# Optimization experiments

Measured on AMD Instinct MI355X. Metric: run time of the kernel, lower is better.

Reference implementation:

```python
import jax, jax.numpy as jnp
import numpy as np

N = 1 << 20        # number of query points
L_HIDDEN = 6       # hidden (64->64) layers, i.e. params[1:-1]
NEG_SLOPE = 0.2    # nn.LeakyReLU(0.2)

# NOTE: nn.Dropout(0.5) is treated in eval mode (identity), the standard
# convention for deterministic correctness baselines.

def _lrelu(x):
    return jnp.where(x >= 0, x, NEG_SLOPE * x)


def setup_inputs() -> dict:
    key = jax.random.key(0)
    ks = jax.random.split(key, 11)
    return {
        "points": jax.random.normal(ks[0], (N, 3), jnp.float32),
        "w0": jax.random.normal(ks[1], (3, 64), jnp.float32),
        "s0": jax.random.normal(ks[2], (64,), jnp.float32),
        "b0": jax.random.normal(ks[3], (64,), jnp.float32),
        "wh": jax.random.normal(ks[4], (L_HIDDEN, 64, 64), jnp.float32),
        "sh": jax.random.normal(ks[5], (L_HIDDEN, 64), jnp.float32),
        "bh": jax.random.normal(ks[6], (L_HIDDEN, 64), jnp.float32),
        "wo": jax.random.normal(ks[7], (64, 1), jnp.float32),
        "so": jax.random.normal(ks[8], (), jnp.float32),
        "bo": jax.random.normal(ks[9], (), jnp.float32),
    }


def reference(points, w0, s0, b0, wh, sh, bh, wo, so, bo):
    # first layer: [N,3] @ [3,64] * scale + bias -> leakyrelu
    x = _lrelu(jnp.matmul(points, w0) * s0 + b0)
    # hidden layers: small static loop over structurally distinct param sets
    for i in range(L_HIDDEN):
        x = _lrelu(jnp.matmul(x, wh[i]) * sh[i] + bh[i])
    # output layer: [N,64] @ [64,1] * scalar + scalar (no activation)
    return jnp.matmul(x, wo) * so + bo
```

## Files before the change

### kernel.cpp

```cpp
#include <hip/hip_runtime.h>


typedef _Float16 half8 __attribute__((ext_vector_type(8)));
typedef _Float16 half2v __attribute__((ext_vector_type(2)));
typedef float floatx16 __attribute__((ext_vector_type(16)));
typedef float float2v __attribute__((ext_vector_type(2)));

#define N_HID 6
#define OFF_A 0
#define OFF_B 49152
#define OFF_C 51200
#define OFF_D 52992
#define SETUP_TOTAL (24576 + 1024 + 448 + 64)

__global__ __launch_bounds__(256) void setup_weights(
    const float* __restrict__ w0, const float* __restrict__ s0, const float* __restrict__ b0,
    const float* __restrict__ wh, const float* __restrict__ sh, const float* __restrict__ bh,
    const float* __restrict__ wo, const float* __restrict__ so,
    unsigned char* __restrict__ ws)
{
    int i = blockIdx.x * 256 + threadIdx.x;
    if (i < 24576) {
        int j = i & 7, lane = (i >> 3) & 63, s = (i >> 9) & 3, t = (i >> 11) & 1, l = i >> 12;
        int m = 32 * t + (lane & 31);
        int h = lane >> 5;
        int feat = 16 * s + 8 * (j >> 2) + 4 * h + (j & 3);
        ((_Float16*)(ws + OFF_A))[i] = (_Float16)(wh[(l * 64 + feat) * 64 + m] * sh[l * 64 + m]);
    } else if (i < 24576 + 1024) {
        int i2 = i - 24576;
        int j = i2 & 7, lane = (i2 >> 3) & 63, t = i2 >> 9;
        int m = 32 * t + (lane & 31);
        int k = 8 * (lane >> 5) + j;
        float v = (k < 3) ? w0[k * 64 + m] * s0[m] * 0.015625f
                          : (k == 3 ? b0[m] * 0.015625f : 0.f);
        ((_Float16*)(ws + OFF_B))[i2] = (_Float16)v;
    } else if (i < 24576 + 1024 + 448) {
        int i2 = i - 24576 - 1024;
        int r = i2 & 15, t = (i2 >> 4) & 1, h = (i2 >> 5) & 1, l = i2 >> 6;
        int feat = 32 * t + (r & 3) + 8 * ((r >> 2) & 3) + 4 * h;
        float bv = (l == 0) ? b0[feat] : bh[(l - 1) * 64 + feat];
        ((float*)(ws + OFF_C))[i2] = bv * 0.015625f;
    } else if (i < SETUP_TOTAL) {
        int i2 = i - 24576 - 1024 - 448;
        int r = i2 & 15, t = (i2 >> 4) & 1, h = i2 >> 5;
        int feat = 32 * t + (r & 3) + 8 * ((r >> 2) & 3) + 4 * h;
        ((float*)(ws + OFF_D))[i2] = wo[feat] * so[0] * 64.f;
    }
}

union FragU { int i[4]; half8 v; };

static __device__ __forceinline__ int pkrtz(float a, float b) {
    auto hh = __builtin_amdgcn_cvt_pkrtz(a, b);
    int r;
    __builtin_memcpy(&r, &hh, 4);
    return r;
}

static __device__ __forceinline__ int lrelu2(int v) {
    half2v u;
    __builtin_memcpy(&u, &v, 4);
    half2v w = u * (_Float16)0.2f;
    half2v r = __builtin_elementwise_max(u, w);
    int o;
    __builtin_memcpy(&o, &r, 4);
    return o;
}

static __device__ __forceinline__ floatx16 mfma16(half8 a, half8 b, floatx16 c) {
    return __builtin_amdgcn_mfma_f32_32x32x16_f16(a, b, c, 0, 0, 0);
}

__global__ __launch_bounds__(64, 1) void mlp_mfma(
    const float* __restrict__ points,
    const unsigned char* __restrict__ ws,
    const float* __restrict__ bhg,
    const float* __restrict__ bo,
    float* __restrict__ out, int n)
{
    const int lane = threadIdx.x;
    const int p = lane & 31;
    const int h = lane >> 5;

    half8 Wreg[N_HID][2][4];
    {
        const half8* WfG = (const half8*)(ws + OFF_A);
#pragma unroll
        for (int l = 0; l < N_HID; ++l)
#pragma unroll
            for (int t = 0; t < 2; ++t)
#pragma unroll
                for (int s = 0; s < 4; ++s)
                    Wreg[l][t][s] = WfG[(((l * 2 + t) * 4 + s) << 6) + lane];
    }
    half8 W0a, W0b;
    {
        const half8* A0g = (const half8*)(ws + OFF_B);
        W0a = A0g[lane];
        W0b = A0g[64 + lane];
    }
    half8 biasF[N_HID][2];
#pragma unroll
    for (int l = 0; l < N_HID; ++l)
#pragma unroll
        for (int t = 0; t < 2; ++t) {
            FragU u;
            u.i[0] = u.i[1] = u.i[2] = u.i[3] = 0;
            if (h == 0) u.v[0] = (_Float16)(bhg[l * 64 + 32 * t + p] * 0.015625f);
            biasF[l][t] = u.v;
        }
    half8 oneF;
    {
        FragU u;
        u.i[0] = u.i[1] = u.i[2] = u.i[3] = 0;
        if (h == 0) u.v[0] = (_Float16)1.0f;
        oneF = u.v;
    }
    floatx16 wo0, wo1;
    {
        const floatx16* woG = (const floatx16*)(ws + OFF_D);
        wo0 = woG[h * 2 + 0];
        wo1 = woG[h * 2 + 1];
    }
    const float bov = bo[0];

    const int nbatch = (n + 63) >> 6;
    int b = blockIdx.x;
    if (b >= nbatch) return;

    float P0x, P0y, P0z, P1x, P1y, P1z;
    {
        int q0 = min(b * 64 + p, n - 1), q1 = min(b * 64 + 32 + p, n - 1);
        P0x = points[3 * q0]; P0y = points[3 * q0 + 1]; P0z = points[3 * q0 + 2];
        P1x = points[3 * q1]; P1y = points[3 * q1 + 1]; P1z = points[3 * q1 + 2];
    }

    while (true) {
        const int nb = b + (int)gridDim.x;
        const bool more = nb < nbatch;
        float N0x, N0y, N0z, N1x, N1y, N1z;
        N0x = N0y = N0z = N1x = N1y = N1z = 0.f;
        if (more) {
            int q0 = min(nb * 64 + p, n - 1), q1 = min(nb * 64 + 32 + p, n - 1);
            N0x = points[3 * q0]; N0y = points[3 * q0 + 1]; N0z = points[3 * q0 + 2];
            N1x = points[3 * q1]; N1y = points[3 * q1 + 1]; N1z = points[3 * q1 + 2];
        }

        floatx16 acc0[2], acc1[2];
        {
            FragU bu0, bu1;
            bu0.i[0] = bu0.i[1] = bu0.i[2] = bu0.i[3] = 0;
            bu1 = bu0;
            if (h == 0) {
                bu0.v[0] = (_Float16)P0x; bu0.v[1] = (_Float16)P0y;
                bu0.v[2] = (_Float16)P0z; bu0.v[3] = (_Float16)1.0f;
                bu1.v[0] = (_Float16)P1x; bu1.v[1] = (_Float16)P1y;
                bu1.v[2] = (_Float16)P1z; bu1.v[3] = (_Float16)1.0f;
            }
            acc0[0] = mfma16(W0a, bu0.v, (floatx16)(0.0f));
            acc0[1] = mfma16(W0b, bu0.v, (floatx16)(0.0f));
            acc1[0] = mfma16(W0a, bu1.v, (floatx16)(0.0f));
            acc1[1] = mfma16(W0b, bu1.v, (floatx16)(0.0f));
        }

#pragma unroll
        for (int l = 0; l < N_HID; ++l) {
            floatx16 bc0 = mfma16(biasF[l][0], oneF, (floatx16)(0.0f));
            floatx16 bc1 = mfma16(biasF[l][1], oneF, (floatx16)(0.0f));
            floatx16 n00, n01, n10, n11;
#pragma unroll
            for (int s = 0; s < 4; ++s) {
                const int t = s >> 1, rpb = 4 * (s & 1);
                FragU f0, f1;
#pragma unroll
                for (int c = 0; c < 4; ++c) {
                    f0.i[c] = lrelu2(pkrtz(acc0[t][2 * (rpb + c)], acc0[t][2 * (rpb + c) + 1]));
                    f1.i[c] = lrelu2(pkrtz(acc1[t][2 * (rpb + c)], acc1[t][2 * (rpb + c) + 1]));
                }
                if (s == 0) {
                    n00 = mfma16(Wreg[l][0][0], f0.v, bc0);
                    n01 = mfma16(Wreg[l][1][0], f0.v, bc1);
                    n10 = mfma16(Wreg[l][0][0], f1.v, bc0);
                    n11 = mfma16(Wreg[l][1][0], f1.v, bc1);
                } else {
                    n00 = mfma16(Wreg[l][0][s], f0.v, n00);
                    n01 = mfma16(Wreg[l][1][s], f0.v, n01);
                    n10 = mfma16(Wreg[l][0][s], f1.v, n10);
                    n11 = mfma16(Wreg[l][1][s], f1.v, n11);
                }
            }
            acc0[0] = n00; acc0[1] = n01; acc1[0] = n10; acc1[1] = n11;
        }

        {
            float2v q0 = {0.f, 0.f}, q1 = {0.f, 0.f};
#pragma unroll
            for (int r2 = 0; r2 < 8; ++r2) {
                float2v w0p = { wo0[2 * r2], wo0[2 * r2 + 1] };
                float2v w1p = { wo1[2 * r2], wo1[2 * r2 + 1] };
                float2v u;
                u.x = acc0[0][2 * r2]; u.y = acc0[0][2 * r2 + 1];
                u = __builtin_elementwise_max(u, 0.2f * u);
                q0 += u * w0p;
                u.x = acc0[1][2 * r2]; u.y = acc0[1][2 * r2 + 1];
                u = __builtin_elementwise_max(u, 0.2f * u);
                q0 += u * w1p;
                u.x = acc1[0][2 * r2]; u.y = acc1[0][2 * r2 + 1];
                u = __builtin_elementwise_max(u, 0.2f * u);
                q1 += u * w0p;
                u.x = acc1[1][2 * r2]; u.y = acc1[1][2 * r2 + 1];
                u = __builtin_elementwise_max(u, 0.2f * u);
                q1 += u * w1p;
            }
            float part0 = q0.x + q0.y;
            float part1 = q1.x + q1.y;
            part0 += __shfl_xor(part0, 32);
            part1 += __shfl_xor(part1, 32);
            if (h == 0) {
                int pt0 = b * 64 + p, pt1 = b * 64 + 32 + p;
                if (pt0 < n) out[pt0] = part0 + bov;
                if (pt1 < n) out[pt1] = part1 + bov;
            }
        }

        if (!more) break;
        P0x = N0x; P0y = N0y; P0z = N0z;
        P1x = N1x; P1y = N1y; P1z = N1z;
        b = nb;
    }
}

extern "C" void kernel_launch(void* const* d_in, const int* in_sizes, int n_in,
                              void* d_out, int out_size, void* d_ws, size_t ws_size,
                              hipStream_t stream) {
    const float* points = (const float*)d_in[0];
    const float* w0     = (const float*)d_in[1];
    const float* s0     = (const float*)d_in[2];
    const float* b0     = (const float*)d_in[3];
    const float* wh     = (const float*)d_in[4];
    const float* sh     = (const float*)d_in[5];
    const float* bh     = (const float*)d_in[6];
    const float* wo     = (const float*)d_in[7];
    const float* so     = (const float*)d_in[8];
    const float* bo     = (const float*)d_in[9];

    const int n = in_sizes[0] / 3;

    setup_weights<<<(SETUP_TOTAL + 255) / 256, 256, 0, stream>>>(
        w0, s0, b0, wh, sh, bh, wo, so, (unsigned char*)d_ws);

    mlp_mfma<<<1024, 64, 0, stream>>>(
        points, (const unsigned char*)d_ws, bh, bo, (float*)d_out, n);
}
```

Baseline: 143.2 us.

## Pack hidden biases into two MFMA fragments and run two waves per SIMD

Replaces the twelve per-layer bias fragments held in registers with two packed fp16 fragments built in setup, one element per layer. Each layer selects its bias column through a one-hot B fragment in the bias MFMA. This frees VGPRs so launch bounds can ask for two waves per SIMD, and the grid doubles to 2048 blocks to fill them. The risk is register pressure or spills with the tighter bound, since all hidden-layer weights stay resident in registers.

Measured after the change: 199.8 us. 39.6% more time.

```diff
diff --git a/kernel.cpp b/kernel.cpp
--- a/kernel.cpp
+++ b/kernel.cpp
@@ -9,9 +9,9 @@
 #define N_HID 6
 #define OFF_A 0
 #define OFF_B 49152
-#define OFF_C 51200
-#define OFF_D 52992
-#define SETUP_TOTAL (24576 + 1024 + 448 + 64)
+#define OFF_E 51200
+#define OFF_D 53248
+#define SETUP_TOTAL (24576 + 1024 + 1024 + 64)
 
 __global__ __launch_bounds__(256) void setup_weights(
     const float* __restrict__ w0, const float* __restrict__ s0, const float* __restrict__ b0,
@@ -34,14 +34,15 @@
         float v = (k < 3) ? w0[k * 64 + m] * s0[m] * 0.015625f
                           : (k == 3 ? b0[m] * 0.015625f : 0.f);
         ((_Float16*)(ws + OFF_B))[i2] = (_Float16)v;
-    } else if (i < 24576 + 1024 + 448) {
+    } else if (i < 24576 + 2048) {
         int i2 = i - 24576 - 1024;
-        int r = i2 & 15, t = (i2 >> 4) & 1, h = (i2 >> 5) & 1, l = i2 >> 6;
-        int feat = 32 * t + (r & 3) + 8 * ((r >> 2) & 3) + 4 * h;
-        float bv = (l == 0) ? b0[feat] : bh[(l - 1) * 64 + feat];
-        ((float*)(ws + OFF_C))[i2] = bv * 0.015625f;
+        int j = i2 & 7, lane = (i2 >> 3) & 63, t = i2 >> 9;
+        int m = 32 * t + (lane & 31);
+        int h = lane >> 5;
+        float v = (h == 0 && j < N_HID) ? bh[j * 64 + m] * 0.015625f : 0.f;
+        ((_Float16*)(ws + OFF_E))[i2] = (_Float16)v;
     } else if (i < SETUP_TOTAL) {
-        int i2 = i - 24576 - 1024 - 448;
+        int i2 = i - 24576 - 2048;
         int r = i2 & 15, t = (i2 >> 4) & 1, h = i2 >> 5;
         int feat = 32 * t + (r & 3) + 8 * ((r >> 2) & 3) + 4 * h;
         ((float*)(ws + OFF_D))[i2] = wo[feat] * so[0] * 64.f;
@@ -71,10 +72,9 @@
     return __builtin_amdgcn_mfma_f32_32x32x16_f16(a, b, c, 0, 0, 0);
 }
 
-__global__ __launch_bounds__(64, 1) void mlp_mfma(
+__global__ __launch_bounds__(64, 2) void mlp_mfma(
     const float* __restrict__ points,
     const unsigned char* __restrict__ ws,
-    const float* __restrict__ bhg,
     const float* __restrict__ bo,
     float* __restrict__ out, int n)
 {
@@ -99,22 +99,11 @@
         W0a = A0g[lane];
         W0b = A0g[64 + lane];
     }
-    half8 biasF[N_HID][2];
-#pragma unroll
-    for (int l = 0; l < N_HID; ++l)
-#pragma unroll
-        for (int t = 0; t < 2; ++t) {
-            FragU u;
-            u.i[0] = u.i[1] = u.i[2] = u.i[3] = 0;
-            if (h == 0) u.v[0] = (_Float16)(bhg[l * 64 + 32 * t + p] * 0.015625f);
-            biasF[l][t] = u.v;
-        }
-    half8 oneF;
-    {
-        FragU u;
-        u.i[0] = u.i[1] = u.i[2] = u.i[3] = 0;
-        if (h == 0) u.v[0] = (_Float16)1.0f;
-        oneF = u.v;
+    half8 biasAll0, biasAll1;
+    {
+        const half8* Eg = (const half8*)(ws + OFF_E);
+        biasAll0 = Eg[lane];
+        biasAll1 = Eg[64 + lane];
     }
     floatx16 wo0, wo1;
     {
@@ -165,8 +154,11 @@
 
 #pragma unroll
         for (int l = 0; l < N_HID; ++l) {
-            floatx16 bc0 = mfma16(biasF[l][0], oneF, (floatx16)(0.0f));
-            floatx16 bc1 = mfma16(biasF[l][1], oneF, (floatx16)(0.0f));
+            FragU e;
+            e.i[0] = e.i[1] = e.i[2] = e.i[3] = 0;
+            if (h == 0) e.i[l >> 1] = (l & 1) ? 0x3C000000 : 0x00003C00;
+            floatx16 bc0 = mfma16(biasAll0, e.v, (floatx16)(0.0f));
+            floatx16 bc1 = mfma16(biasAll1, e.v, (floatx16)(0.0f));
             floatx16 n00, n01, n10, n11;
 #pragma unroll
             for (int s = 0; s < 4; ++s) {
@@ -249,6 +241,6 @@
     setup_weights<<<(SETUP_TOTAL + 255) / 256, 256, 0, stream>>>(
         w0, s0, b0, wh, sh, bh, wo, so, (unsigned char*)d_ws);
 
-    mlp_mfma<<<1024, 64, 0, stream>>>(
-        points, (const unsigned char*)d_ws, bh, bo, (float*)d_out, n);
-}
+    mlp_mfma<<<2048, 64, 0, stream>>>(
+        points, (const unsigned char*)d_ws, bo, (float*)d_out, n);
+}
```
